# Optimization experiments

Hardware: AMD Instinct MI355X
Metric: run time of the kernel (lower is better)

Reference implementation:

```python
import jax, jax.numpy as jnp
import numpy as np

B, NMAX, NPOOL = 4, 128, 16
I_CNN, QDIM, LIN, NCLS = 2048, 1024, 1024, 16
D_BOX = I_CNN + 4            # 2052: box feat + 4 coords
D_IN = 2 * D_BOX + QDIM      # 5128: g1/g2 first-layer input width


def _make_pool_coords():
    # mirrors RN.make_coords(4): 4x4 grid of boxes over a 448px image, normalized
    W = 448.0
    box = W / 4.0
    c = []
    for y in range(4):
        for x in range(4):
            c.append([x * box, y * box, (x + 1) * box, (y + 1) * box])
    return jnp.asarray(np.array(c) / 448.0, dtype=jnp.float32)


def setup_inputs() -> dict:
    key = jax.random.key(0)
    ks = jax.random.split(key, 32)
    f32 = jnp.float32
    def p(k, shape):
        return jax.random.normal(k, shape, f32) * 0.02
    inp = {
        "wholefeat": jax.random.normal(ks[0], (B, I_CNN), f32),
        "pooled": jax.random.normal(ks[1], (B, NPOOL, I_CNN), f32),
        "box_feats": jax.random.normal(ks[2], (B, NMAX, I_CNN), f32),
        "q_feats": jax.random.normal(ks[3], (B, QDIM), f32),  # q_rnn output (QRNN external)
        "box_coords": jax.random.uniform(ks[4], (B, NMAX, 4), f32),
        "index": jax.random.randint(ks[5], (B,), 16, NMAX + 1),
        # g1 MLP (5128 -> 1024 -> 1024 -> 1024)
        "g1_w1": p(ks[6], (D_IN, LIN)), "g1_b1": jnp.zeros((LIN,), f32),
        "g1_w2": p(ks[7], (LIN, LIN)), "g1_b2": jnp.zeros((LIN,), f32),
        "g1_w3": p(ks[8], (LIN, LIN)), "g1_b3": jnp.zeros((LIN,), f32),
        "f1_w": p(ks[9], (LIN, LIN)), "f1_b": jnp.zeros((LIN,), f32),
        # g2 MLP (5128 -> 1024 -> 1024 -> 1024)
        "g2_w1": p(ks[10], (D_IN, LIN)), "g2_b1": jnp.zeros((LIN,), f32),
        "g2_w2": p(ks[11], (LIN, LIN)), "g2_b2": jnp.zeros((LIN,), f32),
        "g2_w3": p(ks[12], (LIN, LIN)), "g2_b3": jnp.zeros((LIN,), f32),
        "f2_w": p(ks[13], (LIN, LIN)), "f2_b": jnp.zeros((LIN,), f32),
        # fgamma (2048 -> 1024 -> Ncls)
        "fg_w1": p(ks[14], (2 * LIN, 1024)), "fg_b1": jnp.zeros((1024,), f32),
        "fg_w2": p(ks[15], (1024, NCLS)), "fg_b2": jnp.zeros((NCLS,), f32),
        "pool_coords": _make_pool_coords(),
    }
    return inp


def _forward(wholefeat, pooled, box_feats, q_feats, box_coords,
             g1_w1, g1_b1, g1_w2, g1_b2, g1_w3, g1_b3, f1_w, f1_b,
             g2_w1, g2_b1, g2_w2, g2_b2, g2_w3, g2_b3, f2_w, f2_b,
             fg_w1, fg_b1, fg_w2, fg_b2, pool_coords, index):
    relu = jax.nn.relu
    # Decompose first Linear of each g-MLP: cat([b_i, b_j, q]) @ W == b_i@Wa + b_j@Wb + q@Wq
    # (mathematically identical, avoids materializing the [N*N, 5128] concat)
    W1a, W1b, W1q = g1_w1[:D_BOX], g1_w1[D_BOX:2 * D_BOX], g1_w1[2 * D_BOX:]
    W2a, W2b, W2q = g2_w1[:D_BOX], g2_w1[D_BOX:2 * D_BOX], g2_w1[2 * D_BOX:]

    def per_sample(bf, bc, q, pool_i, n):
        # bf: [NMAX, 2048], bc: [NMAX, 4], q: [1024], pool_i: [NPOOL, 2048], n: scalar int
        valid = (jnp.arange(NMAX) < n).astype(bf.dtype)  # ragged mask over boxes
        bfc = jnp.concatenate([bf, bc], axis=-1)          # [NMAX, 2052]
        # g1: all-pairs relation MLP, summed over valid (i, j) pairs
        hq = q @ W1q + g1_b1                              # [1024]
        h = relu((bfc @ W1a)[:, None, :] + (bfc @ W1b)[None, :, :] + hq)  # [NMAX, NMAX, 1024]
        h = relu(h @ g1_w2 + g1_b2)
        h = relu(h @ g1_w3 + g1_b3)
        g1_sum = jnp.einsum('ijd,i,j->d', h, valid, valid)
        rno = relu(g1_sum @ f1_w + f1_b)                  # [1024]
        # g2: box x pooled-grid relation MLP, summed over valid i and all 16 pooled cells
        pc = jnp.concatenate([pool_i, pool_coords], axis=-1)  # [NPOOL, 2052]
        h2 = relu((bfc @ W2a)[:, None, :] + (pc @ W2b)[None, :, :] + (q @ W2q + g2_b1))  # [NMAX, NPOOL, 1024]
        h2 = relu(h2 @ g2_w2 + g2_b2)
        h2 = relu(h2 @ g2_w3 + g2_b3)
        g2_sum = jnp.einsum('ipd,i->d', h2, valid)
        rnob = relu(g2_sum @ f2_w + f2_b)                 # [1024]
        rn = jnp.concatenate([rno, rnob])                 # [2048]
        return relu(rn @ fg_w1 + fg_b1) @ fg_w2 + fg_b2   # [NCLS]

    return jax.vmap(per_sample)(box_feats, box_coords, q_feats, pooled, index)


def reference(wholefeat, pooled, box_feats, q_feats, box_coords,
              g1_w1, g1_b1, g1_w2, g1_b2, g1_w3, g1_b3, f1_w, f1_b,
              g2_w1, g2_b1, g2_w2, g2_b2, g2_w3, g2_b3, f2_w, f2_b,
              fg_w1, fg_b1, fg_w2, fg_b2, pool_coords, index):
    return _forward(wholefeat, pooled, box_feats, q_feats, box_coords,
                    g1_w1, g1_b1, g1_w2, g1_b2, g1_w3, g1_b3, f1_w, f1_b,
                    g2_w1, g2_b1, g2_w2, g2_b2, g2_w3, g2_b3, f2_w, f2_b,
                    fg_w1, fg_b1, fg_w2, fg_b2, pool_coords, index)
```

## Files before the change

kernel.cpp:

```cpp
#include <hip/hip_runtime.h>

typedef __attribute__((ext_vector_type(8))) short short8;
typedef __attribute__((ext_vector_type(8))) __bf16 bf16x8;
typedef __attribute__((ext_vector_type(4))) float f32x4;

__device__ __forceinline__ short f2bf(float f) {
    union { float f; unsigned u; } x; x.f = f;
    unsigned r = (x.u + 0x7FFFu + ((x.u >> 16) & 1u)) >> 16;
    return (short)r;
}

__device__ __forceinline__ f32x4 mfma16(bf16x8 a, bf16x8 b, f32x4 c) {
    return __builtin_amdgcn_mfma_f32_16x16x32_bf16(a, b, c, 0, 0, 0);
}

__device__ __forceinline__ int swz(int slot) { return slot ^ ((slot >> 4) & 7); }

struct WConvP {
    const float* src0[8];
    const float* srcq[8];
    const float* bias[8];
    short*       dst[8];
    int          n0[8];
    int          nK[8];
    int          perm[8];
};

__global__ __launch_bounds__(256) void k_wconv(WConvP P) {
    int y = blockIdx.y;
    int nK = P.nK[y];
    int nchunks = nK << 6;
    int c = blockIdx.x * 4 + (threadIdx.x >> 6);
    if (c >= nchunks) return;
    int l = threadIdx.x & 63;
    int t = c % nK, nf = c / nK;
    int k0 = (t << 5) + ((l >> 4) << 3);
    int n  = (nf << 4) + (l & 15);
    const float* src0 = P.src0[y];
    const float* srcq = P.srcq[y];
    const float* bias = P.bias[y];
    int n0 = P.n0[y], pm = P.perm[y];
    short8 v;
#pragma unroll
    for (int j = 0; j < 8; ++j) {
        int kk = k0 + j;
        float f = 0.f;
        if (pm) {
            int pr = (kk & ~63) | ((kk & 3) << 4) | ((kk >> 2) & 15);
            f = src0[(size_t)pr * 1024 + n];
        } else if (kk < n0) {
            f = src0[(size_t)kk * 1024 + n];
        } else if (srcq && kk >= 2080 && kk < 3104) {
            f = srcq[(size_t)(kk - 2080) * 1024 + n];
        } else if (bias && kk == 3104) {
            f = bias[n];
        }
        v[j] = f2bf(f);
    }
    ((short8*)P.dst[y])[(size_t)c * 64 + l] = v;
}

__global__ __launch_bounds__(256) void k_build(const float* box_feats, const float* box_coords,
                                               const float* pooled, const float* pool_coords,
                                               const float* q_feats, short* bfcq, short* pc) {
    int id = blockIdx.x * 256 + threadIdx.x;
    if (blockIdx.y == 0) {
        if (id >= 512 * 3136) return;
        int row = id / 3136, kp = id - row * 3136;
        int b = row >> 7, i = row & 127;
        float v = 0.f;
        if (kp < 2048)       v = box_feats[((size_t)(b * 128 + i)) * 2048 + kp];
        else if (kp < 2052)  v = box_coords[(b * 128 + i) * 4 + (kp - 2048)];
        else if (kp >= 2080 && kp < 3104) v = q_feats[b * 1024 + (kp - 2080)];
        else if (kp == 3104) v = 1.0f;
        bfcq[id] = f2bf(v);
    } else {
        if (id >= 64 * 2080) return;
        int row = id / 2080, kp = id - row * 2080;
        int b = row >> 4, j = row & 15;
        float v = 0.f;
        if (kp < 2048)      v = pooled[((size_t)(b * 16 + j)) * 2048 + kp];
        else if (kp < 2052) v = pool_coords[j * 4 + (kp - 2048)];
        pc[id] = f2bf(v);
    }
}

struct S1P {
    const short*  X[4];
    const short8* Wf[4];
    float*        Out[4];
    int           xstr[4];
    int           nK[4];
};

__global__ __launch_bounds__(256) void k_stage1(S1P P) {
    int bid = blockIdx.x;
    int z, idx;
    if (bid < 64)       { z = 0; idx = bid; }
    else if (bid < 128) { z = 1; idx = bid - 64; }
    else if (bid < 192) { z = 2; idx = bid - 128; }
    else                { z = 3; idx = bid - 192; }
    int mt = idx >> 2, panel = idx & 3;
    int m0 = mt << 5;
    const short*  Xg = P.X[z];
    const short8* Wf = P.Wf[z];
    float* Out = P.Out[z];
    int xstr = P.xstr[z], nK = P.nK[z];

    int tid = threadIdx.x, w = tid >> 6, l = tid & 63, lr = l & 15, lh = l >> 4;
    int nfb = (panel << 4) + (w << 2);
    const short8* Wl = Wf + (size_t)nfb * nK * 64 + l;
    f32x4 z4 = {0.f, 0.f, 0.f, 0.f};
    f32x4 acc[2][4];
#pragma unroll
    for (int mf = 0; mf < 2; ++mf)
#pragma unroll
        for (int f = 0; f < 4; ++f) acc[mf][f] = z4;

    for (int t = 0; t < nK; ++t) {
        int k0 = (t << 5) + (lh << 3);
        const short* xb = Xg + (size_t)(m0 + lr) * xstr + k0;
        bf16x8 a0 = __builtin_bit_cast(bf16x8, *(const short8*)xb);
        bf16x8 a1 = __builtin_bit_cast(bf16x8, *(const short8*)(xb + (size_t)16 * xstr));
#pragma unroll
        for (int f = 0; f < 4; ++f) {
            bf16x8 bb = __builtin_bit_cast(bf16x8, Wl[((size_t)f * nK + t) << 6]);
            acc[0][f] = mfma16(a0, bb, acc[0][f]);
            acc[1][f] = mfma16(a1, bb, acc[1][f]);
        }
    }
#pragma unroll
    for (int mf = 0; mf < 2; ++mf)
#pragma unroll
        for (int f = 0; f < 4; ++f)
#pragma unroll
            for (int r = 0; r < 4; ++r) {
                int row = m0 + (mf << 4) + (lh << 2) + r;
                int col = (panel << 8) + (w << 6) + (f << 4) + lr;
                Out[(size_t)row * 1024 + col] = acc[mf][f][r];
            }
}

struct FuseP {
    const float*  Arow;
    const float*  Brow;
    const short8* W2;
    const short8* W3;
    const float*  b2;
    const float*  b3;
    float*        gsum;
    const int*    index;
    int           mode;
};

__global__ __launch_bounds__(1024) void k_fused(FuseP P) {
    __shared__ short8 XL[8192];
    int b  = blockIdx.y;
    int nv = P.index[b];
    int npairs = P.mode ? (nv << 4) : (nv * nv);
    int p0 = blockIdx.x << 6;
    if (p0 >= npairs) return;
    int tid = threadIdx.x, w = tid >> 6, l = tid & 63, lr = l & 15, lh = l >> 4;
    const float* Arow = P.Arow + (size_t)b * 128 * 1024;
    const float* Brow = P.Brow + (size_t)b * (P.mode ? 16 : 128) * 1024;

    {
        int mfp = w >> 2;
        int p = p0 + (mfp << 4) + lr;
        int i = 0, j = 0;
        if (p < npairs) {
            if (P.mode) { i = p >> 4; j = p & 15; }
            else        { i = (int)((unsigned)p / (unsigned)nv); j = p - i * nv; }
        }
        const float* Ap = Arow + (size_t)i * 1024;
        const float* Bp = Brow + (size_t)j * 1024;
        int tbase = (w & 3) << 3;
#pragma unroll
        for (int cc = 0; cc < 8; ++cc) {
            int t = tbase + cc;
            int k0 = (t << 5) + (lh << 3);
            f32x4 a0 = *(const f32x4*)(Ap + k0), a1 = *(const f32x4*)(Ap + k0 + 4);
            f32x4 b0 = *(const f32x4*)(Bp + k0), b1 = *(const f32x4*)(Bp + k0 + 4);
            short8 v;
#pragma unroll
            for (int e = 0; e < 4; ++e) {
                v[e]     = f2bf(fmaxf(a0[e] + b0[e], 0.f));
                v[4 + e] = f2bf(fmaxf(a1[e] + b1[e], 0.f));
            }
            XL[swz((((mfp << 5) + t) << 6) + l)] = v;
        }
    }
    float b2l[4], b3l[4];
#pragma unroll
    for (int f = 0; f < 4; ++f) {
        int n = (w << 6) + (f << 4) + lr;
        b2l[f] = P.b2[n];
        b3l[f] = P.b3[n];
    }
    __syncthreads();

    const short8* W2l = P.W2 + ((size_t)w << 13) + l;
    f32x4 z4 = {0.f, 0.f, 0.f, 0.f};
    f32x4 acc[4][4];
#pragma unroll
    for (int mf = 0; mf < 4; ++mf)
#pragma unroll
        for (int f = 0; f < 4; ++f) acc[mf][f] = z4;
    for (int t = 0; t < 32; ++t) {
        bf16x8 a[4];
#pragma unroll
        for (int mf = 0; mf < 4; ++mf)
            a[mf] = __builtin_bit_cast(bf16x8, XL[swz((((mf << 5) + t) << 6) + l)]);
#pragma unroll
        for (int f = 0; f < 4; ++f) {
            bf16x8 bb = __builtin_bit_cast(bf16x8, W2l[((f << 5) + t) << 6]);
#pragma unroll
            for (int mf = 0; mf < 4; ++mf)
                acc[mf][f] = mfma16(a[mf], bb, acc[mf][f]);
        }
    }
    __syncthreads();

    {
        unsigned long long* Y8 = (unsigned long long*)XL;
        int t2  = (w << 1) + (lr >> 3);
        int lh2 = (lr >> 1) & 3;
        int half = lr & 1;
#pragma unroll
        for (int mf = 0; mf < 4; ++mf)
#pragma unroll
            for (int r = 0; r < 4; ++r) {
                unsigned long long pk = 0;
#pragma unroll
                for (int f = 0; f < 4; ++f) {
                    unsigned short h = (unsigned short)f2bf(fmaxf(acc[mf][f][r] + b2l[f], 0.f));
                    pk |= (unsigned long long)h << (16 * f);
                }
                int lr2 = (lh << 2) + r;
                int slot = (((mf << 5) + t2) << 6) + (lh2 << 4) + lr2;
                Y8[(swz(slot) << 1) + half] = pk;
            }
    }
    __syncthreads();

    const short8* W3l = P.W3 + ((size_t)w << 13) + l;
#pragma unroll
    for (int mf = 0; mf < 4; ++mf)
#pragma unroll
        for (int f = 0; f < 4; ++f) acc[mf][f] = z4;
    for (int t = 0; t < 32; ++t) {
        bf16x8 a[4];
#pragma unroll
        for (int mf = 0; mf < 4; ++mf)
            a[mf] = __builtin_bit_cast(bf16x8, XL[swz((((mf << 5) + t) << 6) + l)]);
#pragma unroll
        for (int f = 0; f < 4; ++f) {
            bf16x8 bb = __builtin_bit_cast(bf16x8, W3l[((f << 5) + t) << 6]);
#pragma unroll
            for (int mf = 0; mf < 4; ++mf)
                acc[mf][f] = mfma16(a[mf], bb, acc[mf][f]);
        }
    }

#pragma unroll
    for (int f = 0; f < 4; ++f) {
        float s = 0.f;
#pragma unroll
        for (int mf = 0; mf < 4; ++mf)
#pragma unroll
            for (int r = 0; r < 4; ++r) {
                int m = (mf << 4) + (lh << 2) + r;
                if (p0 + m < npairs) s += fmaxf(acc[mf][f][r] + b3l[f], 0.f);
            }
        s += __shfl_xor(s, 16);
        s += __shfl_xor(s, 32);
        if (l < 16) atomicAdd(&P.gsum[(size_t)b * 1024 + (w << 6) + (f << 4) + l], s);
    }
}

__global__ __launch_bounds__(256) void k_t1(const float* g1s, const float* g2s,
                                            const float* f1_w, const float* f1_b,
                                            const float* f2_w, const float* f2_b,
                                            float* rn) {
    __shared__ float red[256];
    int bi = blockIdx.x;
    int s = bi >> 6, b = (bi >> 4) & 3, nb = bi & 15;
    int t = threadIdx.x, nl = t & 63, sl = t >> 6;
    int n = (nb << 6) + nl;
    const float* vin = (s ? g2s : g1s) + b * 1024;
    const float* W = s ? f2_w : f1_w;
    float p = 0.f;
    int k0 = sl << 8;
    for (int k = 0; k < 256; ++k) p += vin[k0 + k] * W[(size_t)(k0 + k) * 1024 + n];
    red[t] = p;
    __syncthreads();
    if (t < 64) {
        float tot = red[t] + red[t + 64] + red[t + 128] + red[t + 192];
        const float* bias = s ? f2_b : f1_b;
        int nn = (nb << 6) + t;
        rn[(size_t)b * 2048 + (s << 10) + nn] = fmaxf(tot + bias[nn], 0.f);
    }
}

__global__ __launch_bounds__(256) void k_t2(const float* rn, const float* fg_w1,
                                            const float* fg_b1, float* u) {
    __shared__ float red[256];
    int bi = blockIdx.x;
    int b = bi >> 4, nb = bi & 15;
    int t = threadIdx.x, nl = t & 63, sl = t >> 6;
    int n = (nb << 6) + nl;
    float p = 0.f;
    int k0 = sl << 9;
    for (int k = 0; k < 512; ++k) p += rn[(size_t)b * 2048 + k0 + k] * fg_w1[(size_t)(k0 + k) * 1024 + n];
    red[t] = p;
    __syncthreads();
    if (t < 64) {
        float tot = red[t] + red[t + 64] + red[t + 128] + red[t + 192];
        int nn = (nb << 6) + t;
        u[(size_t)b * 1024 + nn] = fmaxf(tot + fg_b1[nn], 0.f);
    }
}

__global__ __launch_bounds__(256) void k_t3(const float* u, const float* fg_w2,
                                            const float* fg_b2, float* out) {
    __shared__ float red[256];
    int b = blockIdx.x;
    int t = threadIdx.x, c = t & 15, sl = t >> 4;
    float p = 0.f;
    int k0 = sl << 6;
    for (int k = 0; k < 64; ++k) p += u[(size_t)b * 1024 + k0 + k] * fg_w2[(size_t)(k0 + k) * 16 + c];
    red[t] = p;
    __syncthreads();
    if (t < 16) {
        float tot = 0.f;
#pragma unroll
        for (int s2 = 0; s2 < 16; ++s2) tot += red[t + (s2 << 4)];
        out[b * 16 + t] = tot + fg_b2[t];
    }
}

extern "C" void kernel_launch(void* const* d_in, const int* in_sizes, int n_in,
                              void* d_out, int out_size, void* d_ws, size_t ws_size,
                              hipStream_t stream) {
    (void)in_sizes; (void)n_in; (void)out_size; (void)ws_size;
    const float* pooled      = (const float*)d_in[1];
    const float* box_feats   = (const float*)d_in[2];
    const float* q_feats     = (const float*)d_in[3];
    const float* box_coords  = (const float*)d_in[4];
    const int*   index       = (const int*)d_in[5];
    const float* g1_w1 = (const float*)d_in[6];
    const float* g1_b1 = (const float*)d_in[7];
    const float* g1_w2 = (const float*)d_in[8];
    const float* g1_b2 = (const float*)d_in[9];
    const float* g1_w3 = (const float*)d_in[10];
    const float* g1_b3 = (const float*)d_in[11];
    const float* f1_w  = (const float*)d_in[12];
    const float* f1_b  = (const float*)d_in[13];
    const float* g2_w1 = (const float*)d_in[14];
    const float* g2_b1 = (const float*)d_in[15];
    const float* g2_w2 = (const float*)d_in[16];
    const float* g2_b2 = (const float*)d_in[17];
    const float* g2_w3 = (const float*)d_in[18];
    const float* g2_b3 = (const float*)d_in[19];
    const float* f2_w  = (const float*)d_in[20];
    const float* f2_b  = (const float*)d_in[21];
    const float* fg_w1 = (const float*)d_in[22];
    const float* fg_b1 = (const float*)d_in[23];
    const float* fg_w2 = (const float*)d_in[24];
    const float* fg_b2 = (const float*)d_in[25];
    const float* pool_coords = (const float*)d_in[26];
    float* out = (float*)d_out;

    char* base = (char*)d_ws;
    size_t off = 0;
    auto alloc = [&](size_t bytes) -> void* {
        void* p = base + off;
        off = (off + bytes + 255) & ~(size_t)255;
        return p;
    };
    const size_t szWf98 = (size_t)98 * 64 * 64 * 16;
    const size_t szWf65 = (size_t)65 * 64 * 64 * 16;
    const size_t szWf32 = (size_t)32 * 64 * 64 * 16;
    short* WfA   = (short*)alloc(szWf98);
    short* WfB   = (short*)alloc(szWf65);
    short* Wf2A  = (short*)alloc(szWf98);
    short* Wf2B  = (short*)alloc(szWf65);
    short* Wg1w2 = (short*)alloc(szWf32);
    short* Wg1w3 = (short*)alloc(szWf32);
    short* Wg2w2 = (short*)alloc(szWf32);
    short* Wg2w3 = (short*)alloc(szWf32);
    short* bfcq  = (short*)alloc((size_t)512 * 3136 * 2);
    short* pc    = (short*)alloc((size_t)64 * 2080 * 2);
    float* A1    = (float*)alloc((size_t)512 * 1024 * 4);
    float* B1    = (float*)alloc((size_t)512 * 1024 * 4);
    float* A2    = (float*)alloc((size_t)512 * 1024 * 4);
    float* P2    = (float*)alloc((size_t)64 * 1024 * 4);
    float* sums  = (float*)alloc((size_t)2 * 4096 * 4);
    float* g1s   = sums;
    float* g2s   = sums + 4096;
    float* rn    = (float*)alloc((size_t)4 * 2048 * 4);
    float* u     = (float*)alloc((size_t)4 * 1024 * 4);

    hipMemsetAsync(sums, 0, 2 * 4096 * 4, stream);

    WConvP wp;
    for (int y = 0; y < 8; ++y) { wp.srcq[y] = nullptr; wp.bias[y] = nullptr; wp.perm[y] = 0; }
    wp.src0[0] = g1_w1;                      wp.srcq[0] = g1_w1 + (size_t)4104*1024; wp.bias[0] = g1_b1;
    wp.dst[0] = WfA;   wp.n0[0] = 2052; wp.nK[0] = 98;
    wp.src0[1] = g1_w1 + (size_t)2052*1024;  wp.dst[1] = WfB;   wp.n0[1] = 2052; wp.nK[1] = 65;
    wp.src0[2] = g2_w1;                      wp.srcq[2] = g2_w1 + (size_t)4104*1024; wp.bias[2] = g2_b1;
    wp.dst[2] = Wf2A;  wp.n0[2] = 2052; wp.nK[2] = 98;
    wp.src0[3] = g2_w1 + (size_t)2052*1024;  wp.dst[3] = Wf2B;  wp.n0[3] = 2052; wp.nK[3] = 65;
    wp.src0[4] = g1_w2; wp.dst[4] = Wg1w2; wp.n0[4] = 1024; wp.nK[4] = 32;
    wp.src0[5] = g1_w3; wp.dst[5] = Wg1w3; wp.n0[5] = 1024; wp.nK[5] = 32; wp.perm[5] = 1;
    wp.src0[6] = g2_w2; wp.dst[6] = Wg2w2; wp.n0[6] = 1024; wp.nK[6] = 32;
    wp.src0[7] = g2_w3; wp.dst[7] = Wg2w3; wp.n0[7] = 1024; wp.nK[7] = 32; wp.perm[7] = 1;
    k_wconv<<<dim3(1568, 8), 256, 0, stream>>>(wp);

    k_build<<<dim3(6272, 2), 256, 0, stream>>>(box_feats, box_coords, pooled, pool_coords,
                                               q_feats, bfcq, pc);

    S1P sp;
    sp.X[0] = bfcq; sp.Wf[0] = (const short8*)WfA;  sp.Out[0] = A1; sp.xstr[0] = 3136; sp.nK[0] = 98;
    sp.X[1] = bfcq; sp.Wf[1] = (const short8*)WfB;  sp.Out[1] = B1; sp.xstr[1] = 3136; sp.nK[1] = 65;
    sp.X[2] = bfcq; sp.Wf[2] = (const short8*)Wf2A; sp.Out[2] = A2; sp.xstr[2] = 3136; sp.nK[2] = 98;
    sp.X[3] = pc;   sp.Wf[3] = (const short8*)Wf2B; sp.Out[3] = P2; sp.xstr[3] = 2080; sp.nK[3] = 65;
    k_stage1<<<200, 256, 0, stream>>>(sp);

    FuseP f1p;
    f1p.Arow = A1; f1p.Brow = B1;
    f1p.W2 = (const short8*)Wg1w2; f1p.W3 = (const short8*)Wg1w3;
    f1p.b2 = g1_b2; f1p.b3 = g1_b3; f1p.gsum = g1s; f1p.index = index; f1p.mode = 0;
    k_fused<<<dim3(256, 4), 1024, 0, stream>>>(f1p);

    FuseP f2p;
    f2p.Arow = A2; f2p.Brow = P2;
    f2p.W2 = (const short8*)Wg2w2; f2p.W3 = (const short8*)Wg2w3;
    f2p.b2 = g2_b2; f2p.b3 = g2_b3; f2p.gsum = g2s; f2p.index = index; f2p.mode = 1;
    k_fused<<<dim3(32, 4), 1024, 0, stream>>>(f2p);

    k_t1<<<128, 256, 0, stream>>>(g1s, g2s, f1_w, f1_b, f2_w, f2_b, rn);
    k_t2<<<64, 256, 0, stream>>>(rn, fg_w1, fg_b1, u);
    k_t3<<<4, 256, 0, stream>>>(u, fg_w2, fg_b2, out);
}
```

Before: 476.6 us.

## Merge g1/g2 fused MLP launches and double-buffer weight loads with wider warps

Merges the two k_fused launches (g1 pairs and g2 pooled pairs) into one grid, picking the mode from blockIdx.x. Blocks shrink to 512 threads at two blocks per CU, and each wave now owns 128 output columns (8 MFMA column tiles). The weight fragments are double-buffered in registers, with s_setprio raised around the MFMA bursts so global loads overlap compute. The weight permutation and the LDS writeback of the hidden layer change to match the new 8-wide column layout. This raises register pressure, which may limit occupancy or cause spills.

```diff
diff --git a/kernel.cpp b/kernel.cpp
--- a/kernel.cpp
+++ b/kernel.cpp
@@ -46,7 +46,7 @@
         int kk = k0 + j;
         float f = 0.f;
         if (pm) {
-            int pr = (kk & ~63) | ((kk & 3) << 4) | ((kk >> 2) & 15);
+            int pr = (kk & ~127) | ((kk & 7) << 4) | ((kk >> 3) & 15);
             f = src0[(size_t)pr * 1024 + n];
         } else if (kk < n0) {
             f = src0[(size_t)kk * 1024 + n];
@@ -141,42 +141,84 @@
             }
 }
 
+__device__ __forceinline__ void gemm_pipe(const short8* __restrict__ Wl,
+                                          const short8* __restrict__ XLs,
+                                          int l, f32x4 (&acc)[4][8]) {
+    bf16x8 wA[8], wB[8], av[4];
+#pragma unroll
+    for (int f = 0; f < 8; ++f)
+        wA[f] = __builtin_bit_cast(bf16x8, Wl[f << 11]);
+#pragma unroll
+    for (int t = 0; t < 32; t += 2) {
+#pragma unroll
+        for (int f = 0; f < 8; ++f)
+            wB[f] = __builtin_bit_cast(bf16x8, Wl[(f << 11) + ((t + 1) << 6)]);
+#pragma unroll
+        for (int mf = 0; mf < 4; ++mf)
+            av[mf] = __builtin_bit_cast(bf16x8, XLs[swz((((mf << 5) + t) << 6) + l)]);
+        __builtin_amdgcn_s_setprio(1);
+#pragma unroll
+        for (int f = 0; f < 8; ++f)
+#pragma unroll
+            for (int mf = 0; mf < 4; ++mf)
+                acc[mf][f] = mfma16(av[mf], wA[f], acc[mf][f]);
+        __builtin_amdgcn_s_setprio(0);
+        if (t + 2 < 32) {
+#pragma unroll
+            for (int f = 0; f < 8; ++f)
+                wA[f] = __builtin_bit_cast(bf16x8, Wl[(f << 11) + ((t + 2) << 6)]);
+        }
+#pragma unroll
+        for (int mf = 0; mf < 4; ++mf)
+            av[mf] = __builtin_bit_cast(bf16x8, XLs[swz((((mf << 5) + (t + 1)) << 6) + l)]);
+        __builtin_amdgcn_s_setprio(1);
+#pragma unroll
+        for (int f = 0; f < 8; ++f)
+#pragma unroll
+            for (int mf = 0; mf < 4; ++mf)
+                acc[mf][f] = mfma16(av[mf], wB[f], acc[mf][f]);
+        __builtin_amdgcn_s_setprio(0);
+    }
+}
+
 struct FuseP {
-    const float*  Arow;
-    const float*  Brow;
-    const short8* W2;
-    const short8* W3;
-    const float*  b2;
-    const float*  b3;
-    float*        gsum;
+    const float*  Arow[2];
+    const float*  Brow[2];
+    const short8* W2[2];
+    const short8* W3[2];
+    const float*  b2[2];
+    const float*  b3[2];
+    float*        gsum[2];
     const int*    index;
-    int           mode;
 };
 
-__global__ __launch_bounds__(1024) void k_fused(FuseP P) {
+__global__ __launch_bounds__(512, 2) void k_fused(FuseP P) {
     __shared__ short8 XL[8192];
     int b  = blockIdx.y;
+    int px = blockIdx.x;
+    int mode = (px >= 256) ? 1 : 0;
+    int pxl  = mode ? (px - 256) : px;
     int nv = P.index[b];
-    int npairs = P.mode ? (nv << 4) : (nv * nv);
-    int p0 = blockIdx.x << 6;
+    int npairs = mode ? (nv << 4) : (nv * nv);
+    int p0 = pxl << 6;
     if (p0 >= npairs) return;
     int tid = threadIdx.x, w = tid >> 6, l = tid & 63, lr = l & 15, lh = l >> 4;
-    const float* Arow = P.Arow + (size_t)b * 128 * 1024;
-    const float* Brow = P.Brow + (size_t)b * (P.mode ? 16 : 128) * 1024;
+    const float* Arow = P.Arow[mode] + (size_t)b * 128 * 1024;
+    const float* Brow = P.Brow[mode] + (size_t)b * (mode ? 16 : 128) * 1024;
 
     {
-        int mfp = w >> 2;
+        int mfp = w >> 1;
         int p = p0 + (mfp << 4) + lr;
         int i = 0, j = 0;
         if (p < npairs) {
-            if (P.mode) { i = p >> 4; j = p & 15; }
-            else        { i = (int)((unsigned)p / (unsigned)nv); j = p - i * nv; }
+            if (mode) { i = p >> 4; j = p & 15; }
+            else      { i = (int)((unsigned)p / (unsigned)nv); j = p - i * nv; }
         }
         const float* Ap = Arow + (size_t)i * 1024;
         const float* Bp = Brow + (size_t)j * 1024;
-        int tbase = (w & 3) << 3;
-#pragma unroll
-        for (int cc = 0; cc < 8; ++cc) {
+        int tbase = (w & 1) << 4;
+#pragma unroll
+        for (int cc = 0; cc < 16; ++cc) {
             int t = tbase + cc;
             int k0 = (t << 5) + (lh << 3);
             f32x4 a0 = *(const f32x4*)(Ap + k0), a1 = *(const f32x4*)(Ap + k0 + 4);
@@ -190,80 +232,47 @@
             XL[swz((((mfp << 5) + t) << 6) + l)] = v;
         }
     }
-    float b2l[4], b3l[4];
-#pragma unroll
-    for (int f = 0; f < 4; ++f) {
-        int n = (w << 6) + (f << 4) + lr;
-        b2l[f] = P.b2[n];
-        b3l[f] = P.b3[n];
-    }
-    __syncthreads();
-
-    const short8* W2l = P.W2 + ((size_t)w << 13) + l;
+    __syncthreads();
+
     f32x4 z4 = {0.f, 0.f, 0.f, 0.f};
-    f32x4 acc[4][4];
+    f32x4 acc[4][8];
 #pragma unroll
     for (int mf = 0; mf < 4; ++mf)
 #pragma unroll
-        for (int f = 0; f < 4; ++f) acc[mf][f] = z4;
-    for (int t = 0; t < 32; ++t) {
-        bf16x8 a[4];
+        for (int f = 0; f < 8; ++f) acc[mf][f] = z4;
+    gemm_pipe(P.W2[mode] + ((size_t)w << 14) + l, XL, l, acc);
+    __syncthreads();
+
+    {
+        float b2l[8];
+#pragma unroll
+        for (int f = 0; f < 8; ++f) b2l[f] = P.b2[mode][(w << 7) + (f << 4) + lr];
 #pragma unroll
         for (int mf = 0; mf < 4; ++mf)
-            a[mf] = __builtin_bit_cast(bf16x8, XL[swz((((mf << 5) + t) << 6) + l)]);
-#pragma unroll
-        for (int f = 0; f < 4; ++f) {
-            bf16x8 bb = __builtin_bit_cast(bf16x8, W2l[((f << 5) + t) << 6]);
-#pragma unroll
-            for (int mf = 0; mf < 4; ++mf)
-                acc[mf][f] = mfma16(a[mf], bb, acc[mf][f]);
-        }
-    }
-    __syncthreads();
-
-    {
-        unsigned long long* Y8 = (unsigned long long*)XL;
-        int t2  = (w << 1) + (lr >> 3);
-        int lh2 = (lr >> 1) & 3;
-        int half = lr & 1;
-#pragma unroll
-        for (int mf = 0; mf < 4; ++mf)
 #pragma unroll
             for (int r = 0; r < 4; ++r) {
-                unsigned long long pk = 0;
-#pragma unroll
-                for (int f = 0; f < 4; ++f) {
-                    unsigned short h = (unsigned short)f2bf(fmaxf(acc[mf][f][r] + b2l[f], 0.f));
-                    pk |= (unsigned long long)h << (16 * f);
-                }
-                int lr2 = (lh << 2) + r;
-                int slot = (((mf << 5) + t2) << 6) + (lh2 << 4) + lr2;
-                Y8[(swz(slot) << 1) + half] = pk;
+                short8 v;
+#pragma unroll
+                for (int f = 0; f < 8; ++f)
+                    v[f] = f2bf(fmaxf(acc[mf][f][r] + b2l[f], 0.f));
+                int slot = (((mf << 5) + (w << 2) + (lr >> 2)) << 6)
+                         + ((lr & 3) << 4) + (lh << 2) + r;
+                XL[swz(slot)] = v;
             }
     }
     __syncthreads();
 
-    const short8* W3l = P.W3 + ((size_t)w << 13) + l;
 #pragma unroll
     for (int mf = 0; mf < 4; ++mf)
 #pragma unroll
-        for (int f = 0; f < 4; ++f) acc[mf][f] = z4;
-    for (int t = 0; t < 32; ++t) {
-        bf16x8 a[4];
-#pragma unroll
-        for (int mf = 0; mf < 4; ++mf)
-            a[mf] = __builtin_bit_cast(bf16x8, XL[swz((((mf << 5) + t) << 6) + l)]);
-#pragma unroll
-        for (int f = 0; f < 4; ++f) {
-            bf16x8 bb = __builtin_bit_cast(bf16x8, W3l[((f << 5) + t) << 6]);
-#pragma unroll
-            for (int mf = 0; mf < 4; ++mf)
-                acc[mf][f] = mfma16(a[mf], bb, acc[mf][f]);
-        }
-    }
-
-#pragma unroll
-    for (int f = 0; f < 4; ++f) {
+        for (int f = 0; f < 8; ++f) acc[mf][f] = z4;
+    gemm_pipe(P.W3[mode] + ((size_t)w << 14) + l, XL, l, acc);
+
+    float b3l[8];
+#pragma unroll
+    for (int f = 0; f < 8; ++f) b3l[f] = P.b3[mode][(w << 7) + (f << 4) + lr];
+#pragma unroll
+    for (int f = 0; f < 8; ++f) {
         float s = 0.f;
 #pragma unroll
         for (int mf = 0; mf < 4; ++mf)
@@ -274,7 +283,7 @@
             }
         s += __shfl_xor(s, 16);
         s += __shfl_xor(s, 32);
-        if (l < 16) atomicAdd(&P.gsum[(size_t)b * 1024 + (w << 6) + (f << 4) + l], s);
+        if (l < 16) atomicAdd(&P.gsum[mode][(size_t)b * 1024 + (w << 7) + (f << 4) + l], s);
     }
 }
 
@@ -427,17 +436,15 @@
     sp.X[3] = pc;   sp.Wf[3] = (const short8*)Wf2B; sp.Out[3] = P2; sp.xstr[3] = 2080; sp.nK[3] = 65;
     k_stage1<<<200, 256, 0, stream>>>(sp);
 
-    FuseP f1p;
-    f1p.Arow = A1; f1p.Brow = B1;
-    f1p.W2 = (const short8*)Wg1w2; f1p.W3 = (const short8*)Wg1w3;
-    f1p.b2 = g1_b2; f1p.b3 = g1_b3; f1p.gsum = g1s; f1p.index = index; f1p.mode = 0;
-    k_fused<<<dim3(256, 4), 1024, 0, stream>>>(f1p);
-
-    FuseP f2p;
-    f2p.Arow = A2; f2p.Brow = P2;
-    f2p.W2 = (const short8*)Wg2w2; f2p.W3 = (const short8*)Wg2w3;
-    f2p.b2 = g2_b2; f2p.b3 = g2_b3; f2p.gsum = g2s; f2p.index = index; f2p.mode = 1;
-    k_fused<<<dim3(32, 4), 1024, 0, stream>>>(f2p);
+    FuseP fp;
+    fp.Arow[0] = A1; fp.Brow[0] = B1;
+    fp.W2[0] = (const short8*)Wg1w2; fp.W3[0] = (const short8*)Wg1w3;
+    fp.b2[0] = g1_b2; fp.b3[0] = g1_b3; fp.gsum[0] = g1s;
+    fp.Arow[1] = A2; fp.Brow[1] = P2;
+    fp.W2[1] = (const short8*)Wg2w2; fp.W3[1] = (const short8*)Wg2w3;
+    fp.b2[1] = g2_b2; fp.b3[1] = g2_b3; fp.gsum[1] = g2s;
+    fp.index = index;
+    k_fused<<<dim3(288, 4), 512, 0, stream>>>(fp);
 
     k_t1<<<128, 256, 0, stream>>>(g1s, g2s, f1_w, f1_b, f2_w, f2_b, rn);
     k_t2<<<64, 256, 0, stream>>>(rn, fg_w1, fg_b1, u);
```

Result: slower. 489.5 us (+2.7%).
